# Performance work log

Measured on AMD Instinct MI355X. Metric: run time of the kernel, lower is better.

## Reference

```python
import jax, jax.numpy as jnp
import numpy as np

NUM_HEADS = 16
HEAD_DIM = 128
ROT_DIM = 128  # rotary_emb_dim == head_dim
ROPE_BASE = 10000.0


def setup_inputs() -> dict:
    key = jax.random.key(0)
    k1, k2, k3, k4, k5 = jax.random.split(key, 5)
    b, s, d = 2, 2048, 2048
    return {
        "x": jax.random.normal(k1, (b, s, d), jnp.float32),
        "Wqkv_w": jax.random.normal(k2, (3 * d, d), jnp.float32) * (d ** -0.5),
        "Wqkv_b": jax.random.normal(k3, (3 * d,), jnp.float32) * 0.02,
        "wo_w": jax.random.normal(k4, (d, d), jnp.float32) * (d ** -0.5),
        "wo_b": jax.random.normal(k5, (d,), jnp.float32) * 0.02,
    }


def _deinterleave(t):
    # torch.cat([t[..., ::2], t[..., 1::2]], dim=-1)
    return jnp.concatenate([t[..., ::2], t[..., 1::2]], axis=-1)


def _rope(t, cos, sin):
    # non-interleaved (GPT-NeoX style) rotary on first ROT_DIM dims; here ROT_DIM == head_dim
    half = ROT_DIM // 2
    x1, x2 = t[..., :half], t[..., half:ROT_DIM]
    # cos/sin: (s, half) -> broadcast over (b, s, h, half)
    c = cos[None, :, None, :]
    sn = sin[None, :, None, :]
    return jnp.concatenate([x1 * c - x2 * sn, x2 * c + x1 * sn], axis=-1)


def reference(x, Wqkv_w, Wqkv_b, wo_w, wo_b):
    b, s, d = x.shape
    h, hd = NUM_HEADS, HEAD_DIM
    # fused QKV projection, layout '(h three d)' per original rearrange
    qkv = x @ Wqkv_w.T + Wqkv_b                      # (b, s, 3*d)
    qkv = qkv.reshape(b, s, h, 3, hd)
    q = _deinterleave(qkv[:, :, :, 0, :])            # (b, s, h, hd)
    k = _deinterleave(qkv[:, :, :, 1, :])
    v = qkv[:, :, :, 2, :]
    # rotary embedding tables
    inv_freq = 1.0 / (ROPE_BASE ** (jnp.arange(0, ROT_DIM, 2, dtype=jnp.float32) / ROT_DIM))
    freqs = jnp.arange(s, dtype=jnp.float32)[:, None] * inv_freq[None, :]  # (s, half)
    cos, sin = jnp.cos(freqs), jnp.sin(freqs)
    q = _rope(q, cos, sin)
    k = _rope(k, cos, sin)
    # causal self-attention (SelfAttention, softmax_scale = 1/sqrt(hd))
    scale = hd ** -0.5
    scores = jnp.einsum('bshd,bthd->bhst', q, k) * scale  # (b, h, s, s)
    mask = jnp.tril(jnp.ones((s, s), dtype=bool))
    scores = jnp.where(mask[None, None], scores, jnp.finfo(scores.dtype).min)
    probs = jax.nn.softmax(scores, axis=-1)
    ctx = jnp.einsum('bhst,bthd->bshd', probs, v)    # (b, s, h, hd)
    ctx = ctx.reshape(b, s, d)
    return ctx @ wo_w.T + wo_b
```

## Files before the change

### kernel.cpp

```cpp
#include <hip/hip_runtime.h>

#define B_ 2
#define S_ 2048
#define H_ 16
#define HD_ 128
#define QKVROW 6144
#define M_ 4096

typedef float f32x4 __attribute__((ext_vector_type(4)));
typedef __bf16 bf16x8 __attribute__((ext_vector_type(8)));
typedef unsigned short ushortx8 __attribute__((ext_vector_type(8)));

__device__ __forceinline__ float bf2f(unsigned short u) {
  union { unsigned u; float f; } v;
  v.u = ((unsigned)u) << 16;
  return v.f;
}
__device__ __forceinline__ unsigned short f2bf(float f) {
  union { __bf16 b; unsigned short u; } c;
  c.b = (__bf16)f;
  return c.u;
}
__device__ __forceinline__ ushortx8 cvt8(const float* f) {
  const f32x4 lo = *(const f32x4*)f;
  const f32x4 hi = *(const f32x4*)(f + 4);
  ushortx8 o;
#pragma unroll
  for (int t = 0; t < 4; ++t) o[t] = f2bf(lo[t]);
#pragma unroll
  for (int t = 0; t < 4; ++t) o[4 + t] = f2bf(hi[t]);
  return o;
}
__device__ __forceinline__ void async16(const unsigned short* g, unsigned short* l) {
  __builtin_amdgcn_global_load_lds(
      (const __attribute__((address_space(1))) unsigned int*)g,
      (__attribute__((address_space(3))) unsigned int*)l, 16, 0, 0);
}

__global__ __launch_bounds__(256) void f2bf3t(
    const float* __restrict__ a, unsigned short* __restrict__ da, int na8,
    const float* __restrict__ b, unsigned short* __restrict__ db, int nb8,
    const float* __restrict__ c, unsigned short* __restrict__ dc, int nc8,
    float* __restrict__ tab, int nt8) {
  const int ntot = na8 + nb8 + nc8 + nt8;
  int i = blockIdx.x * 256 + threadIdx.x;
  const int stride = gridDim.x * 256;
  for (; i < ntot; i += stride) {
    int off = i;
    if (off < na8 + nb8 + nc8) {
      const float* s;
      unsigned short* d;
      if (off < na8) { s = a; d = da; }
      else if (off - na8 < nb8) { off -= na8; s = b; d = db; }
      else { off -= na8 + nb8; s = c; d = dc; }
      const ushortx8 o = cvt8(s + (size_t)off * 8);
      *(ushortx8*)&d[(size_t)off * 8] = o;
    } else {
      off -= na8 + nb8 + nc8;
      float* dt = tab + (size_t)off * 8;
      const int e0 = off * 8;
      const int s = e0 >> 7;
#pragma unroll
      for (int k = 0; k < 4; ++k) {
        const int j = ((e0 & 127) >> 1) + k;
        const float invf = expf(-(float)j * 0.14391156831212787f);
        float sn, cs;
        sincosf((float)s * invf, &sn, &cs);
        dt[2 * k] = cs;
        dt[2 * k + 1] = sn;
      }
    }
  }
}

__global__ __launch_bounds__(256) void gemm1(
    const unsigned short* __restrict__ A, const unsigned short* __restrict__ Bm,
    const float* __restrict__ bias, unsigned short* __restrict__ C, int mbase) {
  __shared__ unsigned short As[128 * 64];
  __shared__ unsigned short Bs[128 * 64];
  const int tid = threadIdx.x;
  const int lane = tid & 63, wave = tid >> 6;
  const int l15 = lane & 15, quad = lane >> 4;
  const int m0 = mbase + blockIdx.y * 128, n0 = blockIdx.x * 128;
  const int wr = (wave >> 1) * 64, wc = (wave & 1) * 64;

  f32x4 acc[4][4];
#pragma unroll
  for (int r = 0; r < 4; ++r)
#pragma unroll
    for (int c = 0; c < 4; ++c) acc[r][c] = (f32x4){0.f, 0.f, 0.f, 0.f};

  for (int k0 = 0; k0 < 2048; k0 += 64) {
    __syncthreads();
#pragma unroll
    for (int i = 0; i < 4; ++i) {
      const int c0 = wave * 256 + i * 64;
      const int u = c0 + lane;
      const int row = u >> 3, cu = u & 7;
      const int cs = cu ^ (row & 7);
      async16(A + (size_t)(m0 + row) * 2048 + k0 + cs * 8, &As[c0 * 8]);
      async16(Bm + (size_t)(n0 + row) * 2048 + k0 + cs * 8, &Bs[c0 * 8]);
    }
    __syncthreads();

#pragma unroll
    for (int s = 0; s < 2; ++s) {
      bf16x8 af[4], bf[4];
#pragma unroll
      for (int r = 0; r < 4; ++r) {
        const int row = wr + r * 16 + l15;
        af[r] = *(const bf16x8*)&As[row * 64 + (((s * 4 + quad) ^ (row & 7)) << 3)];
      }
#pragma unroll
      for (int c = 0; c < 4; ++c) {
        const int row = wc + c * 16 + l15;
        bf[c] = *(const bf16x8*)&Bs[row * 64 + (((s * 4 + quad) ^ (row & 7)) << 3)];
      }
#pragma unroll
      for (int r = 0; r < 4; ++r)
#pragma unroll
        for (int c = 0; c < 4; ++c)
          acc[r][c] = __builtin_amdgcn_mfma_f32_16x16x32_bf16(af[r], bf[c], acc[r][c], 0, 0, 0);
    }
  }

#pragma unroll
  for (int c = 0; c < 4; ++c) {
    const int col = n0 + wc + c * 16 + l15;
    const float bv = bias[col];
#pragma unroll
    for (int r = 0; r < 4; ++r) {
      const int row = m0 + wr + r * 16 + quad * 4;
#pragma unroll
      for (int i = 0; i < 4; ++i)
        C[(size_t)(row + i) * QKVROW + col] = f2bf(acc[r][c][i] + bv);
    }
  }
}

__global__ __launch_bounds__(256) void rope_vt(
    unsigned short* qkv, unsigned short* __restrict__ Vt,
    const float* __restrict__ tab) {
  __shared__ unsigned short vs[64 * 136];
  const int b = blockIdx.z, h = blockIdx.y, s0 = blockIdx.x * 64;
  const int tid = threadIdx.x;
  const int r = tid >> 2, cpart = (tid & 3) * 32;
  const int s = s0 + r;
  unsigned short* base = qkv + (size_t)(b * S_ + s) * QKVROW + h * 384;
  const int j0 = cpart >> 1;

  ushortx8 ivq[4], ivk[4], ivv[4];
#pragma unroll
  for (int i = 0; i < 4; ++i) {
    ivq[i] = *(const ushortx8*)&base[cpart + i * 8];
    ivk[i] = *(const ushortx8*)&base[128 + cpart + i * 8];
    ivv[i] = *(const ushortx8*)&base[256 + cpart + i * 8];
  }

  float cs[16], sn[16];
  {
    const f32x4* tr = (const f32x4*)&tab[(size_t)s * 128 + j0 * 2];
#pragma unroll
    for (int t = 0; t < 8; ++t) {
      const f32x4 v = tr[t];
      cs[2 * t] = v[0]; sn[2 * t] = v[1];
      cs[2 * t + 1] = v[2]; sn[2 * t + 1] = v[3];
    }
  }

  __syncthreads();

#pragma unroll
  for (int which = 0; which < 2; ++which) {
    const ushortx8* iv = (which == 0) ? ivq : ivk;
    const float scale = (which == 0) ? 0.08838834764831845f : 1.0f;
    ushortx8 o1a, o1b, o2a, o2b;
#pragma unroll
    for (int t = 0; t < 16; ++t) {
      const float x1 = bf2f(iv[(2 * t) >> 3][(2 * t) & 7]);
      const float x2 = bf2f(iv[(2 * t + 1) >> 3][(2 * t + 1) & 7]);
      const unsigned short r1 = f2bf((x1 * cs[t] - x2 * sn[t]) * scale);
      const unsigned short r2 = f2bf((x2 * cs[t] + x1 * sn[t]) * scale);
      if (t < 8) { o1a[t] = r1; o2a[t] = r2; }
      else       { o1b[t - 8] = r1; o2b[t - 8] = r2; }
    }
    unsigned short* out = base + which * 128;
    *(ushortx8*)&out[j0] = o1a;
    *(ushortx8*)&out[j0 + 8] = o1b;
    *(ushortx8*)&out[64 + j0] = o2a;
    *(ushortx8*)&out[64 + j0 + 8] = o2b;
  }

#pragma unroll
  for (int i = 0; i < 4; ++i)
    *(ushortx8*)&vs[r * 136 + cpart + i * 8] = ivv[i];
  __syncthreads();
  const size_t vtb = (size_t)(b * H_ + h) * HD_ * S_ + s0;
#pragma unroll
  for (int it = 0; it < 4; ++it) {
    const int a = tid + it * 256;
    const int d = a >> 3, sc = (a & 7) * 8;
    ushortx8 o;
#pragma unroll
    for (int t = 0; t < 8; ++t) o[t] = vs[(sc + t) * 136 + d];
    *(ushortx8*)&Vt[vtb + (size_t)d * S_ + sc] = o;
  }
}

__global__ __launch_bounds__(256) void attn(
    unsigned short* qkv, const unsigned short* __restrict__ Vt) {
  __shared__ unsigned short Ks[64 * 136];
  __shared__ unsigned short Vs[128 * 72];
  __shared__ unsigned short Ps[4 * 16 * 72];
  const int bh = blockIdx.x, p = blockIdx.y, sub = blockIdx.z;
  const int b = bh >> 4, h = bh & 15;
  const int tid = threadIdx.x, lane = tid & 63, wave = tid >> 6;
  const int l15 = lane & 15, quad = lane >> 4;

  unsigned short* qh = qkv + (size_t)b * S_ * QKVROW + h * 384;
  const unsigned short* Vb = Vt + (size_t)bh * HD_ * S_;
  unsigned short* Pw = &Ps[wave * 16 * 72];

  ushortx8 rk[4], rv[4];
  auto pref = [&](int j) {
#pragma unroll
    for (int t = 0; t < 4; ++t) {
      const int uk = t * 256 + tid;
      const int krow = uk >> 4, kcu = uk & 15;
      rk[t] = *(const ushortx8*)(qh + (size_t)(j * 64 + krow) * QKVROW + 128 + kcu * 8);
      const int vrow = uk >> 3, vcu = uk & 7;
      rv[t] = *(const ushortx8*)(Vb + (size_t)vrow * S_ + j * 64 + vcu * 8);
    }
  };
  pref(0);

#pragma unroll
  for (int half = 0; half < 2; ++half) {
    const int qt = half ? 15 - p : p;
    const int jN = 2 * qt + 1 + sub;
    const int r0 = qt * 128 + sub * 64 + wave * 16;

    bf16x8 aq[4];
#pragma unroll
    for (int ks = 0; ks < 4; ++ks)
      aq[ks] = *(const bf16x8*)&qh[(size_t)(r0 + l15) * QKVROW + ks * 32 + quad * 8];

    f32x4 o[8];
    float mrow[4], lpart[4];
#pragma unroll
    for (int ct = 0; ct < 8; ++ct) o[ct] = (f32x4){0.f, 0.f, 0.f, 0.f};
#pragma unroll
    for (int i = 0; i < 4; ++i) { mrow[i] = -1e30f; lpart[i] = 0.f; }

    for (int j = 0; j < jN; ++j) {
      __syncthreads();
#pragma unroll
      for (int t = 0; t < 4; ++t) {
        const int uk = t * 256 + tid;
        *(ushortx8*)&Ks[(uk >> 4) * 136 + (uk & 15) * 8] = rk[t];
        *(ushortx8*)&Vs[(uk >> 3) * 72 + (uk & 7) * 8] = rv[t];
      }
      __syncthreads();

      const int jn = (j + 1 < jN) ? j + 1 : (half == 0 ? 0 : -1);
      if (jn >= 0) pref(jn);

      f32x4 sacc[4];
#pragma unroll
      for (int ct = 0; ct < 4; ++ct) sacc[ct] = (f32x4){0.f, 0.f, 0.f, 0.f};
      __builtin_amdgcn_s_setprio(1);
#pragma unroll
      for (int ks = 0; ks < 4; ++ks) {
        bf16x8 bk[4];
#pragma unroll
        for (int ct = 0; ct < 4; ++ct)
          bk[ct] = *(const bf16x8*)&Ks[(ct * 16 + l15) * 136 + ks * 32 + quad * 8];
#pragma unroll
        for (int ct = 0; ct < 4; ++ct)
          sacc[ct] = __builtin_amdgcn_mfma_f32_16x16x32_bf16(aq[ks], bk[ct], sacc[ct], 0, 0, 0);
      }
      __builtin_amdgcn_s_setprio(0);

      if (j >= 2 * qt) {
#pragma unroll
        for (int ct = 0; ct < 4; ++ct)
#pragma unroll
          for (int i = 0; i < 4; ++i) {
            const int grow = r0 + quad * 4 + i;
            const int gcol = j * 64 + ct * 16 + l15;
            if (gcol > grow) sacc[ct][i] = -1e30f;
          }
      }

      float tmax[4];
#pragma unroll
      for (int i = 0; i < 4; ++i) {
        float m = fmaxf(fmaxf(sacc[0][i], sacc[1][i]), fmaxf(sacc[2][i], sacc[3][i]));
#pragma unroll
        for (int off = 1; off < 16; off <<= 1) m = fmaxf(m, __shfl_xor(m, off));
        tmax[i] = m;
      }
      bool need = false;
#pragma unroll
      for (int i = 0; i < 4; ++i) need = need || (tmax[i] > mrow[i] + 8.f);
      if (__any(need)) {
#pragma unroll
        for (int i = 0; i < 4; ++i) {
          const float mn = fmaxf(mrow[i], tmax[i]);
          const float alpha = __expf(mrow[i] - mn);
          mrow[i] = mn;
          lpart[i] *= alpha;
#pragma unroll
          for (int ct = 0; ct < 8; ++ct) o[ct][i] *= alpha;
        }
      }
#pragma unroll
      for (int i = 0; i < 4; ++i) {
        float rs = 0.f;
#pragma unroll
        for (int ct = 0; ct < 4; ++ct) {
          const float pv = __expf(sacc[ct][i] - mrow[i]);
          sacc[ct][i] = pv;
          rs += pv;
        }
        lpart[i] += rs;
      }

#pragma unroll
      for (int ct = 0; ct < 4; ++ct)
#pragma unroll
        for (int i = 0; i < 4; ++i)
          Pw[(quad * 4 + i) * 72 + ct * 16 + l15] = f2bf(sacc[ct][i]);

      __builtin_amdgcn_s_setprio(1);
#pragma unroll
      for (int ks = 0; ks < 2; ++ks) {
        const bf16x8 ap = *(const bf16x8*)&Pw[l15 * 72 + ks * 32 + quad * 8];
        bf16x8 bv[8];
#pragma unroll
        for (int ct = 0; ct < 8; ++ct)
          bv[ct] = *(const bf16x8*)&Vs[(ct * 16 + l15) * 72 + ks * 32 + quad * 8];
#pragma unroll
        for (int ct = 0; ct < 8; ++ct)
          o[ct] = __builtin_amdgcn_mfma_f32_16x16x32_bf16(ap, bv[ct], o[ct], 0, 0, 0);
      }
      __builtin_amdgcn_s_setprio(0);
    }

    float inv[4];
#pragma unroll
    for (int i = 0; i < 4; ++i) {
      float l = lpart[i];
#pragma unroll
      for (int off = 1; off < 16; off <<= 1) l += __shfl_xor(l, off);
      inv[i] = 1.0f / l;
    }
#pragma unroll
    for (int ct = 0; ct < 8; ++ct)
#pragma unroll
      for (int i = 0; i < 4; ++i) {
        const int srow = r0 + quad * 4 + i;
        qh[(size_t)srow * QKVROW + ct * 16 + l15] = f2bf(o[ct][i] * inv[i]);
      }
  }
}

__global__ __launch_bounds__(256) void gemm2(
    const unsigned short* __restrict__ A, const unsigned short* __restrict__ Bm,
    const float* __restrict__ bias, float* __restrict__ C) {
  __shared__ unsigned short As[128 * 64];
  __shared__ unsigned short Bs[128 * 64];
  const int tid = threadIdx.x;
  const int lane = tid & 63, wave = tid >> 6;
  const int l15 = lane & 15, quad = lane >> 4;
  const int m0 = blockIdx.y * 128, n0 = blockIdx.x * 128;
  const int wr = (wave >> 1) * 64, wc = (wave & 1) * 64;

  f32x4 acc[4][4];
#pragma unroll
  for (int r = 0; r < 4; ++r)
#pragma unroll
    for (int c = 0; c < 4; ++c) acc[r][c] = (f32x4){0.f, 0.f, 0.f, 0.f};

  for (int k0 = 0; k0 < 2048; k0 += 64) {
    const int kh = ((k0 >> 7) * 384) + (k0 & 127);
    __syncthreads();
#pragma unroll
    for (int i = 0; i < 4; ++i) {
      const int c0 = wave * 256 + i * 64;
      const int u = c0 + lane;
      const int row = u >> 3, cu = u & 7;
      const int cs = cu ^ (row & 7);
      async16(A + (size_t)(m0 + row) * QKVROW + kh + cs * 8, &As[c0 * 8]);
      async16(Bm + (size_t)(n0 + row) * 2048 + k0 + cs * 8, &Bs[c0 * 8]);
    }
    __syncthreads();

#pragma unroll
    for (int s = 0; s < 2; ++s) {
      bf16x8 af[4], bf[4];
#pragma unroll
      for (int r = 0; r < 4; ++r) {
        const int row = wr + r * 16 + l15;
        af[r] = *(const bf16x8*)&As[row * 64 + (((s * 4 + quad) ^ (row & 7)) << 3)];
      }
#pragma unroll
      for (int c = 0; c < 4; ++c) {
        const int row = wc + c * 16 + l15;
        bf[c] = *(const bf16x8*)&Bs[row * 64 + (((s * 4 + quad) ^ (row & 7)) << 3)];
      }
#pragma unroll
      for (int r = 0; r < 4; ++r)
#pragma unroll
        for (int c = 0; c < 4; ++c)
          acc[r][c] = __builtin_amdgcn_mfma_f32_16x16x32_bf16(af[r], bf[c], acc[r][c], 0, 0, 0);
    }
  }

#pragma unroll
  for (int c = 0; c < 4; ++c) {
    const int col = n0 + wc + c * 16 + l15;
    const float bv = bias[col];
#pragma unroll
    for (int r = 0; r < 4; ++r) {
      const int row = m0 + wr + r * 16 + quad * 4;
#pragma unroll
      for (int i = 0; i < 4; ++i)
        C[(size_t)(row + i) * 2048 + col] = acc[r][c][i] + bv;
    }
  }
}

extern "C" void kernel_launch(void* const* d_in, const int* in_sizes, int n_in,
                              void* d_out, int out_size, void* d_ws, size_t ws_size,
                              hipStream_t stream) {
  const float* x    = (const float*)d_in[0];
  const float* wqkv = (const float*)d_in[1];
  const float* bqkv = (const float*)d_in[2];
  const float* wo   = (const float*)d_in[3];
  const float* bo   = (const float*)d_in[4];
  float* out = (float*)d_out;

  unsigned short* qkv = (unsigned short*)d_ws;
  unsigned short* Vt  = qkv + (size_t)M_ * QKVROW;
  unsigned short* xb  = Vt  + (size_t)B_ * H_ * HD_ * S_;
  unsigned short* wb  = xb  + (size_t)M_ * 2048;
  unsigned short* wob = wb  + (size_t)QKVROW * 2048;
  float* tab = (float*)(wob + (size_t)2048 * 2048);

  f2bf3t<<<dim3(2048), 256, 0, stream>>>(x, xb, (M_ * 2048) / 8,
                                         wqkv, wb, (QKVROW * 2048) / 8,
                                         wo, wob, (2048 * 2048) / 8,
                                         tab, (S_ * 128) / 8);

  gemm1<<<dim3(QKVROW / 128, 16), 256, 0, stream>>>(xb, wb, bqkv, qkv, 0);
  gemm1<<<dim3(QKVROW / 128, 16), 256, 0, stream>>>(xb, wb, bqkv, qkv, 2048);
  rope_vt<<<dim3(S_ / 64, H_, B_), 256, 0, stream>>>(qkv, Vt, tab);
  attn<<<dim3(B_ * H_, 8, 2), 256, 0, stream>>>(qkv, Vt);
  gemm2<<<dim3(2048 / 128, M_ / 128), 256, 0, stream>>>(qkv, wob, bo, out);
}
```

Measured before the change: 436.3 us.

## Swizzle attention LDS tiles, use exp2 softmax, merge QKV GEMM launches

The attention kernel's K, V and P shared-memory tiles drop row padding in favour of an XOR swizzle on 16-byte units, which shrinks LDS use and is meant to avoid bank conflicts. The softmax now uses exp2f, with log2(e) folded into the Q scale inside rope, so the exponent takes one fewer multiply. The two half-M gemm1 launches become a single launch over all of M, cutting launch overhead and tail effects. The swizzle index arithmetic adds some integer work per LDS access.

Result: faster. 405.0 us (-7.2%).

```diff
diff --git a/kernel.cpp b/kernel.cpp
--- a/kernel.cpp
+++ b/kernel.cpp
@@ -75,13 +75,13 @@
 
 __global__ __launch_bounds__(256) void gemm1(
     const unsigned short* __restrict__ A, const unsigned short* __restrict__ Bm,
-    const float* __restrict__ bias, unsigned short* __restrict__ C, int mbase) {
+    const float* __restrict__ bias, unsigned short* __restrict__ C) {
   __shared__ unsigned short As[128 * 64];
   __shared__ unsigned short Bs[128 * 64];
   const int tid = threadIdx.x;
   const int lane = tid & 63, wave = tid >> 6;
   const int l15 = lane & 15, quad = lane >> 4;
-  const int m0 = mbase + blockIdx.y * 128, n0 = blockIdx.x * 128;
+  const int m0 = blockIdx.y * 128, n0 = blockIdx.x * 128;
   const int wr = (wave >> 1) * 64, wc = (wave & 1) * 64;
 
   f32x4 acc[4][4];
@@ -173,7 +173,8 @@
 #pragma unroll
   for (int which = 0; which < 2; ++which) {
     const ushortx8* iv = (which == 0) ? ivq : ivk;
-    const float scale = (which == 0) ? 0.08838834764831845f : 1.0f;
+    const float scale =
+        (which == 0) ? (0.08838834764831845f * 1.4426950408889634f) : 1.0f;
     ushortx8 o1a, o1b, o2a, o2b;
 #pragma unroll
     for (int t = 0; t < 16; ++t) {
@@ -209,9 +210,9 @@
 
 __global__ __launch_bounds__(256) void attn(
     unsigned short* qkv, const unsigned short* __restrict__ Vt) {
-  __shared__ unsigned short Ks[64 * 136];
-  __shared__ unsigned short Vs[128 * 72];
-  __shared__ unsigned short Ps[4 * 16 * 72];
+  __shared__ unsigned short Ks[64 * 128];
+  __shared__ unsigned short Vs[128 * 64];
+  __shared__ unsigned short Ps[4 * 16 * 64];
   const int bh = blockIdx.x, p = blockIdx.y, sub = blockIdx.z;
   const int b = bh >> 4, h = bh & 15;
   const int tid = threadIdx.x, lane = tid & 63, wave = tid >> 6;
@@ -219,7 +220,7 @@
 
   unsigned short* qh = qkv + (size_t)b * S_ * QKVROW + h * 384;
   const unsigned short* Vb = Vt + (size_t)bh * HD_ * S_;
-  unsigned short* Pw = &Ps[wave * 16 * 72];
+  unsigned short* Pw = &Ps[wave * 16 * 64];
 
   ushortx8 rk[4], rv[4];
   auto pref = [&](int j) {
@@ -257,8 +258,10 @@
 #pragma unroll
       for (int t = 0; t < 4; ++t) {
         const int uk = t * 256 + tid;
-        *(ushortx8*)&Ks[(uk >> 4) * 136 + (uk & 15) * 8] = rk[t];
-        *(ushortx8*)&Vs[(uk >> 3) * 72 + (uk & 7) * 8] = rv[t];
+        const int krow = uk >> 4, kun = uk & 15;
+        *(ushortx8*)&Ks[krow * 128 + ((kun ^ (krow & 7)) << 3)] = rk[t];
+        const int vrow = uk >> 3, vun = uk & 7;
+        *(ushortx8*)&Vs[vrow * 64 + ((vun ^ (vrow & 7)) << 3)] = rv[t];
       }
       __syncthreads();
 
@@ -274,7 +277,8 @@
         bf16x8 bk[4];
 #pragma unroll
         for (int ct = 0; ct < 4; ++ct)
-          bk[ct] = *(const bf16x8*)&Ks[(ct * 16 + l15) * 136 + ks * 32 + quad * 8];
+          bk[ct] = *(const bf16x8*)&Ks[(ct * 16 + l15) * 128 +
+                                       (((ks * 4 + quad) ^ (l15 & 7)) << 3)];
 #pragma unroll
         for (int ct = 0; ct < 4; ++ct)
           sacc[ct] = __builtin_amdgcn_mfma_f32_16x16x32_bf16(aq[ks], bk[ct], sacc[ct], 0, 0, 0);
@@ -307,7 +311,7 @@
 #pragma unroll
         for (int i = 0; i < 4; ++i) {
           const float mn = fmaxf(mrow[i], tmax[i]);
-          const float alpha = __expf(mrow[i] - mn);
+          const float alpha = exp2f(mrow[i] - mn);
           mrow[i] = mn;
           lpart[i] *= alpha;
 #pragma unroll
@@ -319,7 +323,7 @@
         float rs = 0.f;
 #pragma unroll
         for (int ct = 0; ct < 4; ++ct) {
-          const float pv = __expf(sacc[ct][i] - mrow[i]);
+          const float pv = exp2f(sacc[ct][i] - mrow[i]);
           sacc[ct][i] = pv;
           rs += pv;
         }
@@ -329,17 +333,22 @@
 #pragma unroll
       for (int ct = 0; ct < 4; ++ct)
 #pragma unroll
-        for (int i = 0; i < 4; ++i)
-          Pw[(quad * 4 + i) * 72 + ct * 16 + l15] = f2bf(sacc[ct][i]);
+        for (int i = 0; i < 4; ++i) {
+          const int row = quad * 4 + i;
+          const int u = ct * 2 + (l15 >> 3);
+          Pw[row * 64 + ((u ^ (row & 7)) << 3) + (l15 & 7)] = f2bf(sacc[ct][i]);
+        }
 
       __builtin_amdgcn_s_setprio(1);
 #pragma unroll
       for (int ks = 0; ks < 2; ++ks) {
-        const bf16x8 ap = *(const bf16x8*)&Pw[l15 * 72 + ks * 32 + quad * 8];
+        const bf16x8 ap = *(const bf16x8*)&Pw[l15 * 64 +
+                                              (((ks * 4 + quad) ^ (l15 & 7)) << 3)];
         bf16x8 bv[8];
 #pragma unroll
         for (int ct = 0; ct < 8; ++ct)
-          bv[ct] = *(const bf16x8*)&Vs[(ct * 16 + l15) * 72 + ks * 32 + quad * 8];
+          bv[ct] = *(const bf16x8*)&Vs[(ct * 16 + l15) * 64 +
+                                       (((ks * 4 + quad) ^ (l15 & 7)) << 3)];
 #pragma unroll
         for (int ct = 0; ct < 8; ++ct)
           o[ct] = __builtin_amdgcn_mfma_f32_16x16x32_bf16(ap, bv[ct], o[ct], 0, 0, 0);
@@ -453,8 +462,7 @@
                                          wo, wob, (2048 * 2048) / 8,
                                          tab, (S_ * 128) / 8);
 
-  gemm1<<<dim3(QKVROW / 128, 16), 256, 0, stream>>>(xb, wb, bqkv, qkv, 0);
-  gemm1<<<dim3(QKVROW / 128, 16), 256, 0, stream>>>(xb, wb, bqkv, qkv, 2048);
+  gemm1<<<dim3(QKVROW / 128, M_ / 128), 256, 0, stream>>>(xb, wb, bqkv, qkv);
   rope_vt<<<dim3(S_ / 64, H_, B_), 256, 0, stream>>>(qkv, Vt, tab);
   attn<<<dim3(B_ * H_, 8, 2), 256, 0, stream>>>(qkv, Vt);
   gemm2<<<dim3(2048 / 128, M_ / 128), 256, 0, stream>>>(qkv, wob, bo, out);
```
